# Kernel optimization log

Hardware: AMD Instinct MI355X
Metric: run time of the kernel (lower is better)

Reference implementation:

```python
import jax, jax.numpy as jnp
import numpy as np

N = 50000   # nodes
E = 800000  # edges (avg out-degree 16)
F = 64      # node features
HID = 128   # hidden size


def _seg(vals, idx, n):
    return jax.ops.segment_sum(vals, idx, num_segments=n)


def dconv(x, src, dst, nw_out, nw_in, W, b, n):
    # Diffusion convolution, K=2. W: (2, K, C, HID); directions: out-walk / in-walk.
    # k=0 term is the identity hop for both directions.
    h = x @ (W[0, 0] + W[1, 0])
    fwd = _seg(nw_out[:, None] * x[src], dst, n)  # (D_out^-1 A) x
    bwd = _seg(nw_in[:, None] * x[dst], src, n)   # (D_in^-1 A^T) x
    return h + fwd @ W[0, 1] + bwd @ W[1, 1] + b


def dcrnn_cell(x, src, dst, nw_out, nw_in, Wz, bz, Wr, br, Wh, bh, n, hid):
    # Single recurrent step with H initialized to zeros (as in the model's single-call use).
    h0 = jnp.zeros((x.shape[0], hid), x.dtype)
    xh = jnp.concatenate([x, h0], axis=-1)
    z = jax.nn.sigmoid(dconv(xh, src, dst, nw_out, nw_in, Wz, bz, n))
    r = jax.nn.sigmoid(dconv(xh, src, dst, nw_out, nw_in, Wr, br, n))
    xrh = jnp.concatenate([x, r * h0], axis=-1)
    h_tilde = jnp.tanh(dconv(xrh, src, dst, nw_out, nw_in, Wh, bh, n))
    return z * h0 + (1.0 - z) * h_tilde


def setup_inputs() -> dict:
    key = jax.random.key(0)
    ks = jax.random.split(key, 20)
    x = jax.random.normal(ks[0], (N, F), jnp.float32)
    edge_index = jax.random.randint(ks[1], (2, E), 0, N, jnp.int32)
    edge_weight = jax.random.uniform(ks[2], (E,), jnp.float32)

    c1 = F + HID
    c2 = HID + HID

    def mkW(k, c):
        return jax.random.normal(k, (2, 2, c, HID), jnp.float32) / np.float32(np.sqrt(c))

    inp = {
        "x": x,
        "edge_index": edge_index,
        "edge_weight": edge_weight,
        "W1_z": mkW(ks[3], c1), "b1_z": jnp.zeros((HID,), jnp.float32),
        "W1_r": mkW(ks[4], c1), "b1_r": jnp.zeros((HID,), jnp.float32),
        "W1_h": mkW(ks[5], c1), "b1_h": jnp.zeros((HID,), jnp.float32),
        "W2_z": mkW(ks[6], c2), "b2_z": jnp.zeros((HID,), jnp.float32),
        "W2_r": mkW(ks[7], c2), "b2_r": jnp.zeros((HID,), jnp.float32),
        "W2_h": mkW(ks[8], c2), "b2_h": jnp.zeros((HID,), jnp.float32),
        "Wlin": jax.random.normal(ks[9], (HID, 1), jnp.float32) / np.float32(np.sqrt(HID)),
        "blin": jnp.zeros((1,), jnp.float32),
    }
    return inp


def reference(x, edge_index, edge_weight,
              W1_z, b1_z, W1_r, b1_r, W1_h, b1_h,
              W2_z, b2_z, W2_r, b2_r, W2_h, b2_h,
              Wlin, blin):
    src, dst = edge_index[0], edge_index[1]
    n = x.shape[0]
    # Random-walk normalization of edge weights (out- and in-degree), safe reciprocal.
    deg_out = _seg(edge_weight, src, n)
    deg_in = _seg(edge_weight, dst, n)
    nw_out = edge_weight * jnp.where(deg_out[src] > 0, 1.0 / deg_out[src], 0.0)
    nw_in = edge_weight * jnp.where(deg_in[dst] > 0, 1.0 / deg_in[dst], 0.0)

    h = dcrnn_cell(x, src, dst, nw_out, nw_in, W1_z, b1_z, W1_r, b1_r, W1_h, b1_h, n, HID)
    h = dcrnn_cell(h, src, dst, nw_out, nw_in, W2_z, b2_z, W2_r, b2_r, W2_h, b2_h, n, HID)
    # dropout=0.0 -> identity; final linear head -> (N, 1)
    return h @ Wlin + blin
```

## Files before the change

### kernel.cpp

```cpp
#include <hip/hip_runtime.h>
#include <cstdint>
#include <type_traits>

#define NN 50000
#define NE 800000
#define CAP 48
#define NPART 391
#define BINCAP 2560
#define CHUNK 4096

typedef unsigned short u16;
typedef unsigned int u32;
typedef unsigned long long u64;
typedef u16 u16x8 __attribute__((ext_vector_type(8)));
typedef __bf16 bf16x8 __attribute__((ext_vector_type(8)));
typedef float f32x4 __attribute__((ext_vector_type(4)));

__device__ __forceinline__ u16 f2bf(float f) {
  u32 u = __float_as_uint(f);
  u = (u + 0x7fff + ((u >> 16) & 1)) >> 16;
  return (u16)u;
}
__device__ __forceinline__ float bf2f(u32 b) { return __uint_as_float(b << 16); }

__launch_bounds__(512)
__global__ void k_bin(const int* __restrict__ src, const int* __restrict__ dst,
                      const float* __restrict__ ew, int2* __restrict__ bins,
                      u32* __restrict__ binCnt) {
  const int dir = blockIdx.y;
  const int e0 = blockIdx.x * CHUNK;
  const int n = min(CHUNK, NE - e0);
  const int* key = dir ? src : dst;
  const int* oth = dir ? dst : src;
  __shared__ u32 cnt[512];
  __shared__ u32 scan[512];
  __shared__ u32 gbase[512];
  __shared__ int2 ent[CHUNK];
  __shared__ u32 dsts[CHUNK];
  const int t = threadIdx.x;
  cnt[t] = 0;
  __syncthreads();

  int pj[8], mj[8], wj[8];
  u32 oj[8];
#pragma unroll
  for (int j = 0; j < 8; ++j) {
    const int i = j * 512 + t;
    pj[j] = -1;
    if (i < n) {
      const int e = e0 + i;
      const int k = key[e];
      pj[j] = k >> 7;
      mj[j] = ((k & 127) << 16) | oth[e];
      wj[j] = __float_as_int(ew[e]);
      oj[j] = atomicAdd(&cnt[pj[j]], 1u);
    }
  }
  __syncthreads();
  scan[t] = cnt[t];
  __syncthreads();
  for (int s = 1; s < 512; s <<= 1) {
    u32 v = (t >= s) ? scan[t - s] : 0;
    __syncthreads();
    scan[t] += v;
    __syncthreads();
  }
  if (t < NPART) gbase[t] = cnt[t] ? atomicAdd(&binCnt[dir * NPART + t], cnt[t]) : 0;
  __syncthreads();
#pragma unroll
  for (int j = 0; j < 8; ++j) {
    if (pj[j] >= 0) {
      const int p = pj[j];
      const u32 slot = scan[p] - cnt[p] + oj[j];
      ent[slot] = make_int2(mj[j], wj[j]);
      const u32 go = gbase[p] + oj[j];
      dsts[slot] = (go < BINCAP) ? (u32)p * BINCAP + go : 0xFFFFFFFFu;
    }
  }
  __syncthreads();
  int2* bdir = bins + (size_t)dir * NPART * BINCAP;
  for (int i = t; i < n; i += 512) {
    const u32 d = dsts[i];
    if (d != 0xFFFFFFFFu) bdir[d] = ent[i];
  }
}

__launch_bounds__(512)
__global__ void k_scatter2(const int2* __restrict__ bins, const u32* __restrict__ binCnt,
                           int2* __restrict__ bucketF, int2* __restrict__ bucketB,
                           u32* __restrict__ cntNF, u32* __restrict__ cntNB,
                           float* __restrict__ invF, float* __restrict__ invB) {
  const int p = blockIdx.x, dir = blockIdx.y;
  __shared__ u64 cd[128];
  __shared__ int2 stage[128 * CAP];
  const int t = threadIdx.x;
  if (t < 128) cd[t] = 0;
  __syncthreads();
  const int2* bin = bins + ((size_t)dir * NPART + p) * BINCAP;
  int bn = binCnt[dir * NPART + p];
  if (bn > BINCAP) bn = BINCAP;
  for (int i = t; i < bn; i += 512) {
    const int2 e = bin[i];
    const int ln = e.x >> 16;
    const float w = __int_as_float(e.y);
    const u64 inc = (1ULL << 32) | (u64)__float2uint_rn(w * 16777216.0f);
    const u32 slot = (u32)(atomicAdd(&cd[ln], inc) >> 32);
    if (slot < CAP) stage[ln * CAP + slot] = make_int2(e.x & 0xffff, e.y);
  }
  __syncthreads();
  int2* bucket = dir ? bucketB : bucketF;
  for (int i = t; i < 128 * CAP; i += 512) {
    const int ln = i / CAP, s = i % CAP;
    const int g = p * 128 + ln;
    u32 c = (u32)(cd[ln] >> 32);
    if (c > CAP) c = CAP;
    if (g < NN && s < (int)c) bucket[(size_t)g * CAP + s] = stage[i];
  }
  if (t < 128) {
    const int g = p * 128 + t;
    if (g < NN) {
      u32 c = (u32)(cd[t] >> 32);
      const u32 dfix = (u32)cd[t];
      if (c > CAP) c = CAP;
      (dir ? cntNB : cntNF)[g] = c;
      (dir ? invB : invF)[g] = dfix ? 16777216.f / (float)dfix : 0.f;
    }
  }
}

__global__ void k_cast(const float* __restrict__ x, u16* __restrict__ xb) {
  int i = (blockIdx.x * 256 + threadIdx.x) * 8;
  if (i >= NN * 64) return;
  float4 v0 = *(const float4*)&x[i];
  float4 v1 = *(const float4*)&x[i + 4];
  u16x8 o;
  o[0] = f2bf(v0.x); o[1] = f2bf(v0.y); o[2] = f2bf(v0.z); o[3] = f2bf(v0.w);
  o[4] = f2bf(v1.x); o[5] = f2bf(v1.y); o[6] = f2bf(v1.z); o[7] = f2bf(v1.w);
  *(u16x8*)&xb[i] = o;
}

template <int C>
__global__ void k_pack(const float* __restrict__ Wz, const float* __restrict__ Wh,
                       u16* __restrict__ WpT) {
  constexpr int K = 3 * C;
  constexpr int CIN = (C == 64) ? 192 : 256;
  int col = blockIdx.x;
  int k = threadIdx.x;
  int part = k / C, c = k % C, o = col & 127;
  const float* W = (col < 128) ? Wz : Wh;
  float v;
  if (part == 0)      v = W[(0 * CIN + c) * 128 + o] + W[(2 * CIN + c) * 128 + o];
  else if (part == 1) v = W[(1 * CIN + c) * 128 + o];
  else                v = W[(3 * CIN + c) * 128 + o];
  WpT[col * K + k] = f2bf(v);
}

template <int C>
__launch_bounds__(256)
__global__ void k_gather(const u16* __restrict__ x, const u32* __restrict__ cntNF,
                         const int2* __restrict__ bucketF, const u32* __restrict__ cntNB,
                         const int2* __restrict__ bucketB, const float* __restrict__ invF,
                         const float* __restrict__ invB, u16* __restrict__ fwd,
                         u16* __restrict__ bwd) {
  constexpr int G = C / 8;
  constexpr int NG = 64 / G;
  const int node = blockIdx.x * 4 + (threadIdx.x >> 6);
  if (node >= NN) return;
  const int lane = threadIdx.x & 63;
  const int g = lane / G;
  const int p = lane % G;
  const uint4* xa = (const uint4*)x;

  const int nF = cntNF[node];
  const int nB = cntNB[node];

  int2 entF = make_int2(0, 0), entB = make_int2(0, 0);
  if (lane < nF) entF = bucketF[(size_t)node * CAP + lane];
  if (lane < nB) entB = bucketB[(size_t)node * CAP + lane];
  const float wFl = __int_as_float(entF.y) * invB[entF.x];
  const float wBl = __int_as_float(entB.y) * invF[entB.x];

  float accF[8], accB[8];
#pragma unroll
  for (int j = 0; j < 8; ++j) { accF[j] = 0.f; accB[j] = 0.f; }

  const int mm = nF > nB ? nF : nB;
#pragma unroll 2
  for (int i = 0; i < mm; i += NG) {
    const int ii = i + g;
    const int mF = __shfl(entF.x, ii);
    const float wF = __shfl(wFl, ii);
    const int mB = __shfl(entB.x, ii);
    const float wB = __shfl(wBl, ii);
    uint4 vF = {0, 0, 0, 0}, vB = {0, 0, 0, 0};
    if (ii < nF) vF = xa[(u32)mF * G + p];
    if (ii < nB) vB = xa[(u32)mB * G + p];
    accF[0] += wF * bf2f(vF.x & 0xffff); accF[1] += wF * bf2f(vF.x >> 16);
    accF[2] += wF * bf2f(vF.y & 0xffff); accF[3] += wF * bf2f(vF.y >> 16);
    accF[4] += wF * bf2f(vF.z & 0xffff); accF[5] += wF * bf2f(vF.z >> 16);
    accF[6] += wF * bf2f(vF.w & 0xffff); accF[7] += wF * bf2f(vF.w >> 16);
    accB[0] += wB * bf2f(vB.x & 0xffff); accB[1] += wB * bf2f(vB.x >> 16);
    accB[2] += wB * bf2f(vB.y & 0xffff); accB[3] += wB * bf2f(vB.y >> 16);
    accB[4] += wB * bf2f(vB.z & 0xffff); accB[5] += wB * bf2f(vB.z >> 16);
    accB[6] += wB * bf2f(vB.w & 0xffff); accB[7] += wB * bf2f(vB.w >> 16);
  }

#pragma unroll
  for (int s = 32; s >= G; s >>= 1) {
#pragma unroll
    for (int j = 0; j < 8; ++j) {
      accF[j] += __shfl_xor(accF[j], s);
      accB[j] += __shfl_xor(accB[j], s);
    }
  }

  if (g < 2) {
    const float* a = g ? accB : accF;
    u16* o = g ? bwd : fwd;
    u16x8 pv;
#pragma unroll
    for (int j = 0; j < 8; ++j) pv[j] = f2bf(a[j]);
    *(u16x8*)&o[(size_t)node * C + p * 8] = pv;
  }
}

template <int C, bool HEAD>
__launch_bounds__(256)
__global__ void k_gemm(const u16* __restrict__ P0, const u16* __restrict__ P1,
                       const u16* __restrict__ P2, const u16* __restrict__ WpT,
                       const float* __restrict__ bz, const float* __restrict__ bh,
                       void* __restrict__ outv, const float* __restrict__ wlin,
                       const float* __restrict__ blin) {
  constexpr int K = 3 * C;
  __shared__ char smem[40960];
  u16* As = (u16*)smem;
  u16* Bs = (u16*)(smem + 8192);
  const int t = threadIdx.x;
  const int w = t >> 6;
  const int l = t & 63;
  const int lc = l & 15, lq = l >> 4;
  const int bm = blockIdx.x * 64;

  f32x4 acc[4][4];
#pragma unroll
  for (int mi = 0; mi < 4; ++mi)
#pragma unroll
    for (int ni = 0; ni < 4; ++ni) acc[mi][ni] = (f32x4){0.f, 0.f, 0.f, 0.f};

  for (int kt = 0; kt < K / 64; ++kt) {
    const int k0 = kt * 64;
    const u16* P;
    int lc0;
    if (C == 64) { P = (kt == 0) ? P0 : (kt == 1 ? P1 : P2); lc0 = 0; }
    else         { P = (kt < 2) ? P0 : (kt < 4 ? P1 : P2);   lc0 = (kt & 1) * 64; }
    {
      const int row = t >> 2;
      const int gr = bm + row;
      const int g0 = (t & 3) * 2;
      u16x8 v0 = {0, 0, 0, 0, 0, 0, 0, 0}, v1 = v0;
      if (gr < NN) {
        const u16* s = &P[(size_t)gr * C + lc0 + g0 * 8];
        v0 = *(const u16x8*)s;
        v1 = *(const u16x8*)(s + 8);
      }
      *(u16x8*)&As[row * 64 + ((g0 ^ (row & 7)) * 8)] = v0;
      *(u16x8*)&As[row * 64 + (((g0 + 1) ^ (row & 7)) * 8)] = v1;
    }
    {
      const int col = t;
      const u16* s = &WpT[(size_t)col * K + k0];
#pragma unroll
      for (int g = 0; g < 8; ++g) {
        u16x8 v = *(const u16x8*)(s + g * 8);
        *(u16x8*)&Bs[col * 64 + ((g ^ (col & 7)) * 8)] = v;
      }
    }
    __syncthreads();
#pragma unroll
    for (int kk = 0; kk < 2; ++kk) {
      bf16x8 af[4], bfr[4];
#pragma unroll
      for (int mi = 0; mi < 4; ++mi) {
        const int row = 16 * mi + lc;
        const int g = kk * 4 + lq;
        af[mi] = *(const bf16x8*)&As[row * 64 + ((g ^ (row & 7)) * 8)];
      }
#pragma unroll
      for (int ni = 0; ni < 4; ++ni) {
        const int col = 64 * w + 16 * ni + lc;
        const int g = kk * 4 + lq;
        bfr[ni] = *(const bf16x8*)&Bs[col * 64 + ((g ^ (col & 7)) * 8)];
      }
#pragma unroll
      for (int mi = 0; mi < 4; ++mi)
#pragma unroll
        for (int ni = 0; ni < 4; ++ni)
          acc[mi][ni] = __builtin_amdgcn_mfma_f32_16x16x32_bf16(af[mi], bfr[ni],
                                                                acc[mi][ni], 0, 0, 0);
    }
    __syncthreads();
  }

  float* Hs = (float*)smem;
  if (w >= 2) {
#pragma unroll
    for (int mi = 0; mi < 4; ++mi)
#pragma unroll
      for (int ni = 0; ni < 4; ++ni) {
        const int c2 = 64 * (w - 2) + 16 * ni + lc;
        const float bhv = bh[c2];
#pragma unroll
        for (int r = 0; r < 4; ++r)
          Hs[(16 * mi + 4 * lq + r) * 129 + c2] = tanhf(acc[mi][ni][r] + bhv);
      }
  }
  float* outS = (float*)(smem + 33280);
  if (HEAD && t < 64) outS[t] = 0.f;
  __syncthreads();

  if (w < 2) {
    if constexpr (!HEAD) {
      u16* out = (u16*)outv;
#pragma unroll
      for (int mi = 0; mi < 4; ++mi)
#pragma unroll
        for (int ni = 0; ni < 4; ++ni) {
          const int col = 64 * w + 16 * ni + lc;
          const float bzv = bz[col];
#pragma unroll
          for (int r = 0; r < 4; ++r) {
            const int row = 16 * mi + 4 * lq + r;
            const int gr = bm + row;
            const float z = 1.f / (1.f + __expf(-(acc[mi][ni][r] + bzv)));
            const float hv = (1.f - z) * Hs[row * 129 + col];
            if (gr < NN) out[(size_t)gr * 128 + col] = f2bf(hv);
          }
        }
    } else {
#pragma unroll
      for (int mi = 0; mi < 4; ++mi)
#pragma unroll
        for (int r = 0; r < 4; ++r) {
          const int row = 16 * mi + 4 * lq + r;
          float part = 0.f;
#pragma unroll
          for (int ni = 0; ni < 4; ++ni) {
            const int col = 64 * w + 16 * ni + lc;
            const float z = 1.f / (1.f + __expf(-(acc[mi][ni][r] + bz[col])));
            part += (1.f - z) * Hs[row * 129 + col] * wlin[col];
          }
          part += __shfl_xor(part, 1);
          part += __shfl_xor(part, 2);
          part += __shfl_xor(part, 4);
          part += __shfl_xor(part, 8);
          if (lc == 0) atomicAdd(&outS[row], part);
        }
    }
  }
  if constexpr (HEAD) {
    __syncthreads();
    if (t < 64) {
      const int gr = bm + t;
      if (gr < NN) ((float*)outv)[gr] = outS[t] + blin[0];
    }
  }
}

extern "C" void kernel_launch(void* const* d_in, const int* in_sizes, int n_in,
                              void* d_out, int out_size, void* d_ws, size_t ws_size,
                              hipStream_t stream) {
  const float* x    = (const float*)d_in[0];
  const int*   ei   = (const int*)d_in[1];
  const float* ew   = (const float*)d_in[2];
  const float* W1z  = (const float*)d_in[3];
  const float* b1z  = (const float*)d_in[4];
  const float* W1h  = (const float*)d_in[7];
  const float* b1h  = (const float*)d_in[8];
  const float* W2z  = (const float*)d_in[9];
  const float* b2z  = (const float*)d_in[10];
  const float* W2h  = (const float*)d_in[13];
  const float* b2h  = (const float*)d_in[14];
  const float* Wlin = (const float*)d_in[15];
  const float* blin = (const float*)d_in[16];
  const int* src = ei;
  const int* dst = ei + NE;

  char* p8 = (char*)d_ws;
  auto alloc = [&](size_t bytes) { char* r = p8; p8 += (bytes + 15) & ~15ull; return r; };
  u32*   binCnt  = (u32*)alloc(2 * NPART * 4);
  int2*  bins    = (int2*)alloc((size_t)2 * NPART * BINCAP * 8);
  int2*  bucketF = (int2*)alloc((size_t)NN * CAP * 8);
  int2*  bucketB = (int2*)alloc((size_t)NN * CAP * 8);
  u32*   cntNF   = (u32*)alloc(NN * 4);
  u32*   cntNB   = (u32*)alloc(NN * 4);
  float* invF    = (float*)alloc(NN * 4);
  float* invB    = (float*)alloc(NN * 4);
  u16*   WpT1 = (u16*)alloc(256 * 192 * 2);
  u16*   WpT2 = (u16*)alloc(256 * 384 * 2);
  u16*   xb   = (u16*)alloc((size_t)NN * 64 * 2);
  u16*   h1   = (u16*)alloc((size_t)NN * 128 * 2);
  u16*   fwd1 = (u16*)alloc((size_t)NN * 64 * 2);
  u16*   bwd1 = (u16*)alloc((size_t)NN * 64 * 2);
  u16*   bwd2 = (u16*)alloc((size_t)NN * 128 * 2);
  u16*   fwd2 = fwd1;

  hipMemsetAsync(binCnt, 0, 2 * NPART * 4, stream);

  const dim3 binGrid((NE + CHUNK - 1) / CHUNK, 2);
  k_bin<<<binGrid, 512, 0, stream>>>(src, dst, ew, bins, binCnt);
  k_scatter2<<<dim3(NPART, 2), 512, 0, stream>>>(bins, binCnt, bucketF, bucketB,
                                                 cntNF, cntNB, invF, invB);
  k_pack<64><<<256, 192, 0, stream>>>(W1z, W1h, WpT1);
  k_pack<128><<<256, 384, 0, stream>>>(W2z, W2h, WpT2);
  k_cast<<<(NN * 64 / 8 + 255) / 256, 256, 0, stream>>>(x, xb);

  const int nb4 = (NN + 3) / 4;
  const int gblocks = (NN + 63) / 64;

  k_gather<64><<<nb4, 256, 0, stream>>>(xb, cntNF, bucketF, cntNB, bucketB, invF, invB,
                                        fwd1, bwd1);
  k_gemm<64, false><<<gblocks, 256, 0, stream>>>(xb, fwd1, bwd1, WpT1, b1z, b1h, h1,
                                                 nullptr, nullptr);
  k_gather<128><<<nb4, 256, 0, stream>>>(h1, cntNF, bucketF, cntNB, bucketB, invF, invB,
                                         fwd2, bwd2);
  k_gemm<128, true><<<gblocks, 256, 0, stream>>>(h1, fwd2, bwd2, WpT2, b2z, b2h,
                                                 d_out, Wlin, blin);
}
```

Before: 252.3 us.

## Sort gather neighbor lists per node and use persistent grid-stride gather blocks

Each wave now sorts its node's forward and backward neighbor entries by source index with an in-register 64-lane bitonic sort, so the feature-row gathers run in ascending address order for better cache and DRAM locality. Empty lanes are padded with a max key and clamped when indexing the inverse-degree arrays. The gather kernels also switch from one block per four nodes to a fixed grid of 1280 blocks looping over nodes. The sort adds about 21 shuffle stages per direction per node, and the different summation order changes bf16 rounding slightly.

```diff
diff --git a/kernel.cpp b/kernel.cpp
--- a/kernel.cpp
+++ b/kernel.cpp
@@ -8,6 +8,7 @@
 #define NPART 391
 #define BINCAP 2560
 #define CHUNK 4096
+#define NBLK 1280
 
 typedef unsigned short u16;
 typedef unsigned int u32;
@@ -22,6 +23,20 @@
   return (u16)u;
 }
 __device__ __forceinline__ float bf2f(u32 b) { return __uint_as_float(b << 16); }
+
+__device__ __forceinline__ void bitonic64(int& key, int& val, const int lane) {
+#pragma unroll
+  for (int k = 2; k <= 64; k <<= 1) {
+#pragma unroll
+    for (int j = k >> 1; j > 0; j >>= 1) {
+      const int pk = __shfl_xor(key, j);
+      const int pv = __shfl_xor(val, j);
+      const bool keepmin = ((lane & j) == 0) == ((lane & k) == 0);
+      const bool adopt = keepmin ? (pk < key) : (pk > key);
+      if (adopt) { key = pk; val = pv; }
+    }
+  }
+}
 
 __launch_bounds__(512)
 __global__ void k_bin(const int* __restrict__ src, const int* __restrict__ dst,
@@ -164,63 +179,69 @@
                          u16* __restrict__ bwd) {
   constexpr int G = C / 8;
   constexpr int NG = 64 / G;
-  const int node = blockIdx.x * 4 + (threadIdx.x >> 6);
-  if (node >= NN) return;
   const int lane = threadIdx.x & 63;
   const int g = lane / G;
   const int p = lane % G;
   const uint4* xa = (const uint4*)x;
 
-  const int nF = cntNF[node];
-  const int nB = cntNB[node];
-
-  int2 entF = make_int2(0, 0), entB = make_int2(0, 0);
-  if (lane < nF) entF = bucketF[(size_t)node * CAP + lane];
-  if (lane < nB) entB = bucketB[(size_t)node * CAP + lane];
-  const float wFl = __int_as_float(entF.y) * invB[entF.x];
-  const float wBl = __int_as_float(entB.y) * invF[entB.x];
-
-  float accF[8], accB[8];
-#pragma unroll
-  for (int j = 0; j < 8; ++j) { accF[j] = 0.f; accB[j] = 0.f; }
-
-  const int mm = nF > nB ? nF : nB;
+  for (int node = blockIdx.x * 4 + (threadIdx.x >> 6); node < NN; node += NBLK * 4) {
+    const int nF = cntNF[node];
+    const int nB = cntNB[node];
+
+    int2 entF = make_int2(0x7FFFFFFF, 0), entB = make_int2(0x7FFFFFFF, 0);
+    if (lane < nF) entF = bucketF[(size_t)node * CAP + lane];
+    if (lane < nB) entB = bucketB[(size_t)node * CAP + lane];
+
+    bitonic64(entF.x, entF.y, lane);
+    bitonic64(entB.x, entB.y, lane);
+
+    const int ixF = min(entF.x, NN - 1);
+    const int ixB = min(entB.x, NN - 1);
+    const float wFl = __int_as_float(entF.y) * invB[ixF];
+    const float wBl = __int_as_float(entB.y) * invF[ixB];
+
+    float accF[8], accB[8];
+#pragma unroll
+    for (int j = 0; j < 8; ++j) { accF[j] = 0.f; accB[j] = 0.f; }
+
+    const int mm = nF > nB ? nF : nB;
 #pragma unroll 2
-  for (int i = 0; i < mm; i += NG) {
-    const int ii = i + g;
-    const int mF = __shfl(entF.x, ii);
-    const float wF = __shfl(wFl, ii);
-    const int mB = __shfl(entB.x, ii);
-    const float wB = __shfl(wBl, ii);
-    uint4 vF = {0, 0, 0, 0}, vB = {0, 0, 0, 0};
-    if (ii < nF) vF = xa[(u32)mF * G + p];
-    if (ii < nB) vB = xa[(u32)mB * G + p];
-    accF[0] += wF * bf2f(vF.x & 0xffff); accF[1] += wF * bf2f(vF.x >> 16);
-    accF[2] += wF * bf2f(vF.y & 0xffff); accF[3] += wF * bf2f(vF.y >> 16);
-    accF[4] += wF * bf2f(vF.z & 0xffff); accF[5] += wF * bf2f(vF.z >> 16);
-    accF[6] += wF * bf2f(vF.w & 0xffff); accF[7] += wF * bf2f(vF.w >> 16);
-    accB[0] += wB * bf2f(vB.x & 0xffff); accB[1] += wB * bf2f(vB.x >> 16);
-    accB[2] += wB * bf2f(vB.y & 0xffff); accB[3] += wB * bf2f(vB.y >> 16);
-    accB[4] += wB * bf2f(vB.z & 0xffff); accB[5] += wB * bf2f(vB.z >> 16);
-    accB[6] += wB * bf2f(vB.w & 0xffff); accB[7] += wB * bf2f(vB.w >> 16);
-  }
-
-#pragma unroll
-  for (int s = 32; s >= G; s >>= 1) {
-#pragma unroll
-    for (int j = 0; j < 8; ++j) {
-      accF[j] += __shfl_xor(accF[j], s);
-      accB[j] += __shfl_xor(accB[j], s);
-    }
-  }
-
-  if (g < 2) {
-    const float* a = g ? accB : accF;
-    u16* o = g ? bwd : fwd;
-    u16x8 pv;
-#pragma unroll
-    for (int j = 0; j < 8; ++j) pv[j] = f2bf(a[j]);
-    *(u16x8*)&o[(size_t)node * C + p * 8] = pv;
+    for (int i = 0; i < mm; i += NG) {
+      const int ii = i + g;
+      const int mF = __shfl(entF.x, ii);
+      const float wF = __shfl(wFl, ii);
+      const int mB = __shfl(entB.x, ii);
+      const float wB = __shfl(wBl, ii);
+      uint4 vF = {0, 0, 0, 0}, vB = {0, 0, 0, 0};
+      if (ii < nF) vF = xa[(u32)mF * G + p];
+      if (ii < nB) vB = xa[(u32)mB * G + p];
+      accF[0] += wF * bf2f(vF.x & 0xffff); accF[1] += wF * bf2f(vF.x >> 16);
+      accF[2] += wF * bf2f(vF.y & 0xffff); accF[3] += wF * bf2f(vF.y >> 16);
+      accF[4] += wF * bf2f(vF.z & 0xffff); accF[5] += wF * bf2f(vF.z >> 16);
+      accF[6] += wF * bf2f(vF.w & 0xffff); accF[7] += wF * bf2f(vF.w >> 16);
+      accB[0] += wB * bf2f(vB.x & 0xffff); accB[1] += wB * bf2f(vB.x >> 16);
+      accB[2] += wB * bf2f(vB.y & 0xffff); accB[3] += wB * bf2f(vB.y >> 16);
+      accB[4] += wB * bf2f(vB.z & 0xffff); accB[5] += wB * bf2f(vB.z >> 16);
+      accB[6] += wB * bf2f(vB.w & 0xffff); accB[7] += wB * bf2f(vB.w >> 16);
+    }
+
+#pragma unroll
+    for (int s = 32; s >= G; s >>= 1) {
+#pragma unroll
+      for (int j = 0; j < 8; ++j) {
+        accF[j] += __shfl_xor(accF[j], s);
+        accB[j] += __shfl_xor(accB[j], s);
+      }
+    }
+
+    if (g < 2) {
+      const float* a = g ? accB : accF;
+      u16* o = g ? bwd : fwd;
+      u16x8 pv;
+#pragma unroll
+      for (int j = 0; j < 8; ++j) pv[j] = f2bf(a[j]);
+      *(u16x8*)&o[(size_t)node * C + p * 8] = pv;
+    }
   }
 }
 
@@ -414,15 +435,14 @@
   k_pack<128><<<256, 384, 0, stream>>>(W2z, W2h, WpT2);
   k_cast<<<(NN * 64 / 8 + 255) / 256, 256, 0, stream>>>(x, xb);
 
-  const int nb4 = (NN + 3) / 4;
   const int gblocks = (NN + 63) / 64;
 
-  k_gather<64><<<nb4, 256, 0, stream>>>(xb, cntNF, bucketF, cntNB, bucketB, invF, invB,
-                                        fwd1, bwd1);
+  k_gather<64><<<NBLK, 256, 0, stream>>>(xb, cntNF, bucketF, cntNB, bucketB, invF, invB,
+                                         fwd1, bwd1);
   k_gemm<64, false><<<gblocks, 256, 0, stream>>>(xb, fwd1, bwd1, WpT1, b1z, b1h, h1,
                                                  nullptr, nullptr);
-  k_gather<128><<<nb4, 256, 0, stream>>>(h1, cntNF, bucketF, cntNB, bucketB, invF, invB,
-                                         fwd2, bwd2);
+  k_gather<128><<<NBLK, 256, 0, stream>>>(h1, cntNF, bucketF, cntNB, bucketB, invF, invB,
+                                          fwd2, bwd2);
   k_gemm<128, true><<<gblocks, 256, 0, stream>>>(h1, fwd2, bwd2, WpT2, b2z, b2h,
                                                  d_out, Wlin, blin);
 }
```

New measurement: 317.5 us. 25.8% more time.

## Pack bucket entries into 32-bit index+fp16 weight and widen GEMM tile to 128 rows

Applied to the files above, without the earlier changes.

Bucket entries shrink from 8-byte int2 (index, float weight) to a 32-bit word holding a 16-bit local index and an fp16 weight. This halves bucket write and read traffic in the scatter and gather kernels, and the gather now reads buckets with nontemporal loads. The GEMM block tile doubles from 64 to 128 rows, so each B tile load is reused by more MFMAs, with the epilogue run in two 64-row halves. The costs are reduced weight precision, more accumulator registers (possibly lower occupancy), and a larger shared-memory footprint.

```diff
diff --git a/kernel.cpp b/kernel.cpp
--- a/kernel.cpp
+++ b/kernel.cpp
@@ -1,4 +1,5 @@
 #include <hip/hip_runtime.h>
+#include <hip/hip_fp16.h>
 #include <cstdint>
 #include <type_traits>
 
@@ -87,12 +88,12 @@
 
 __launch_bounds__(512)
 __global__ void k_scatter2(const int2* __restrict__ bins, const u32* __restrict__ binCnt,
-                           int2* __restrict__ bucketF, int2* __restrict__ bucketB,
+                           u32* __restrict__ bucketF, u32* __restrict__ bucketB,
                            u32* __restrict__ cntNF, u32* __restrict__ cntNB,
                            float* __restrict__ invF, float* __restrict__ invB) {
   const int p = blockIdx.x, dir = blockIdx.y;
   __shared__ u64 cd[128];
-  __shared__ int2 stage[128 * CAP];
+  __shared__ u32 stage[128 * CAP];
   const int t = threadIdx.x;
   if (t < 128) cd[t] = 0;
   __syncthreads();
@@ -105,10 +106,12 @@
     const float w = __int_as_float(e.y);
     const u64 inc = (1ULL << 32) | (u64)__float2uint_rn(w * 16777216.0f);
     const u32 slot = (u32)(atomicAdd(&cd[ln], inc) >> 32);
-    if (slot < CAP) stage[ln * CAP + slot] = make_int2(e.x & 0xffff, e.y);
-  }
-  __syncthreads();
-  int2* bucket = dir ? bucketB : bucketF;
+    const __half hw = __float2half_rn(w);
+    if (slot < CAP)
+      stage[ln * CAP + slot] = ((u32)(e.x & 0xffff) << 16) | (u32)__half_as_ushort(hw);
+  }
+  __syncthreads();
+  u32* bucket = dir ? bucketB : bucketF;
   for (int i = t; i < 128 * CAP; i += 512) {
     const int ln = i / CAP, s = i % CAP;
     const int g = p * 128 + ln;
@@ -158,8 +161,8 @@
 template <int C>
 __launch_bounds__(256)
 __global__ void k_gather(const u16* __restrict__ x, const u32* __restrict__ cntNF,
-                         const int2* __restrict__ bucketF, const u32* __restrict__ cntNB,
-                         const int2* __restrict__ bucketB, const float* __restrict__ invF,
+                         const u32* __restrict__ bucketF, const u32* __restrict__ cntNB,
+                         const u32* __restrict__ bucketB, const float* __restrict__ invF,
                          const float* __restrict__ invB, u16* __restrict__ fwd,
                          u16* __restrict__ bwd) {
   constexpr int G = C / 8;
@@ -174,11 +177,15 @@
   const int nF = cntNF[node];
   const int nB = cntNB[node];
 
-  int2 entF = make_int2(0, 0), entB = make_int2(0, 0);
-  if (lane < nF) entF = bucketF[(size_t)node * CAP + lane];
-  if (lane < nB) entB = bucketB[(size_t)node * CAP + lane];
-  const float wFl = __int_as_float(entF.y) * invB[entF.x];
-  const float wBl = __int_as_float(entB.y) * invF[entB.x];
+  u32 eF = 0, eB = 0;
+  if (lane < nF) eF = __builtin_nontemporal_load(&bucketF[(size_t)node * CAP + lane]);
+  if (lane < nB) eB = __builtin_nontemporal_load(&bucketB[(size_t)node * CAP + lane]);
+  const int idxF = eF >> 16;
+  const int idxB = eB >> 16;
+  const float wFl =
+      __half2float(__ushort_as_half((u16)(eF & 0xffff))) * invB[idxF];
+  const float wBl =
+      __half2float(__ushort_as_half((u16)(eB & 0xffff))) * invF[idxB];
 
   float accF[8], accB[8];
 #pragma unroll
@@ -188,9 +195,9 @@
 #pragma unroll 2
   for (int i = 0; i < mm; i += NG) {
     const int ii = i + g;
-    const int mF = __shfl(entF.x, ii);
+    const int mF = __shfl(idxF, ii);
     const float wF = __shfl(wFl, ii);
-    const int mB = __shfl(entB.x, ii);
+    const int mB = __shfl(idxB, ii);
     const float wB = __shfl(wBl, ii);
     uint4 vF = {0, 0, 0, 0}, vB = {0, 0, 0, 0};
     if (ii < nF) vF = xa[(u32)mF * G + p];
@@ -232,18 +239,18 @@
                        void* __restrict__ outv, const float* __restrict__ wlin,
                        const float* __restrict__ blin) {
   constexpr int K = 3 * C;
-  __shared__ char smem[40960];
+  __shared__ char smem[49152];
   u16* As = (u16*)smem;
-  u16* Bs = (u16*)(smem + 8192);
+  u16* Bs = (u16*)(smem + 16384);
   const int t = threadIdx.x;
   const int w = t >> 6;
   const int l = t & 63;
   const int lc = l & 15, lq = l >> 4;
-  const int bm = blockIdx.x * 64;
-
-  f32x4 acc[4][4];
-#pragma unroll
-  for (int mi = 0; mi < 4; ++mi)
+  const int bm = blockIdx.x * 128;
+
+  f32x4 acc[8][4];
+#pragma unroll
+  for (int mi = 0; mi < 8; ++mi)
 #pragma unroll
     for (int ni = 0; ni < 4; ++ni) acc[mi][ni] = (f32x4){0.f, 0.f, 0.f, 0.f};
 
@@ -254,17 +261,20 @@
     if (C == 64) { P = (kt == 0) ? P0 : (kt == 1 ? P1 : P2); lc0 = 0; }
     else         { P = (kt < 2) ? P0 : (kt < 4 ? P1 : P2);   lc0 = (kt & 1) * 64; }
     {
-      const int row = t >> 2;
+      const int row = t >> 1;
       const int gr = bm + row;
-      const int g0 = (t & 3) * 2;
-      u16x8 v0 = {0, 0, 0, 0, 0, 0, 0, 0}, v1 = v0;
+      const int g0 = (t & 1) * 4;
+      u16x8 v[4];
+#pragma unroll
+      for (int j = 0; j < 4; ++j) v[j] = (u16x8){0, 0, 0, 0, 0, 0, 0, 0};
       if (gr < NN) {
         const u16* s = &P[(size_t)gr * C + lc0 + g0 * 8];
-        v0 = *(const u16x8*)s;
-        v1 = *(const u16x8*)(s + 8);
-      }
-      *(u16x8*)&As[row * 64 + ((g0 ^ (row & 7)) * 8)] = v0;
-      *(u16x8*)&As[row * 64 + (((g0 + 1) ^ (row & 7)) * 8)] = v1;
+#pragma unroll
+        for (int j = 0; j < 4; ++j) v[j] = *(const u16x8*)(s + j * 8);
+      }
+#pragma unroll
+      for (int j = 0; j < 4; ++j)
+        *(u16x8*)&As[row * 64 + (((g0 + j) ^ (row & 7)) * 8)] = v[j];
     }
     {
       const int col = t;
@@ -278,9 +288,9 @@
     __syncthreads();
 #pragma unroll
     for (int kk = 0; kk < 2; ++kk) {
-      bf16x8 af[4], bfr[4];
-#pragma unroll
-      for (int mi = 0; mi < 4; ++mi) {
+      bf16x8 af[8], bfr[4];
+#pragma unroll
+      for (int mi = 0; mi < 8; ++mi) {
         const int row = 16 * mi + lc;
         const int g = kk * 4 + lq;
         af[mi] = *(const bf16x8*)&As[row * 64 + ((g ^ (row & 7)) * 8)];
@@ -292,7 +302,7 @@
         bfr[ni] = *(const bf16x8*)&Bs[col * 64 + ((g ^ (col & 7)) * 8)];
       }
 #pragma unroll
-      for (int mi = 0; mi < 4; ++mi)
+      for (int mi = 0; mi < 8; ++mi)
 #pragma unroll
         for (int ni = 0; ni < 4; ++ni)
           acc[mi][ni] = __builtin_amdgcn_mfma_f32_16x16x32_bf16(af[mi], bfr[ni],
@@ -302,67 +312,74 @@
   }
 
   float* Hs = (float*)smem;
-  if (w >= 2) {
-#pragma unroll
-    for (int mi = 0; mi < 4; ++mi)
-#pragma unroll
-      for (int ni = 0; ni < 4; ++ni) {
-        const int c2 = 64 * (w - 2) + 16 * ni + lc;
-        const float bhv = bh[c2];
-#pragma unroll
-        for (int r = 0; r < 4; ++r)
-          Hs[(16 * mi + 4 * lq + r) * 129 + c2] = tanhf(acc[mi][ni][r] + bhv);
-      }
-  }
   float* outS = (float*)(smem + 33280);
-  if (HEAD && t < 64) outS[t] = 0.f;
-  __syncthreads();
-
-  if (w < 2) {
-    if constexpr (!HEAD) {
-      u16* out = (u16*)outv;
+#pragma unroll
+  for (int half = 0; half < 2; ++half) {
+    if (w >= 2) {
 #pragma unroll
       for (int mi = 0; mi < 4; ++mi)
 #pragma unroll
         for (int ni = 0; ni < 4; ++ni) {
-          const int col = 64 * w + 16 * ni + lc;
-          const float bzv = bz[col];
+          const int c2 = 64 * (w - 2) + 16 * ni + lc;
+          const float bhv = bh[c2];
+#pragma unroll
+          for (int r = 0; r < 4; ++r)
+            Hs[(16 * mi + 4 * lq + r) * 129 + c2] =
+                tanhf(acc[4 * half + mi][ni][r] + bhv);
+        }
+    }
+    if (HEAD && t < 64) outS[t] = 0.f;
+    __syncthreads();
+
+    if (w < 2) {
+      if constexpr (!HEAD) {
+        u16* out = (u16*)outv;
+#pragma unroll
+        for (int mi = 0; mi < 4; ++mi)
+#pragma unroll
+          for (int ni = 0; ni < 4; ++ni) {
+            const int col = 64 * w + 16 * ni + lc;
+            const float bzv = bz[col];
+#pragma unroll
+            for (int r = 0; r < 4; ++r) {
+              const int row = 16 * mi + 4 * lq + r;
+              const int gr = bm + 64 * half + row;
+              const float z =
+                  1.f / (1.f + __expf(-(acc[4 * half + mi][ni][r] + bzv)));
+              const float hv = (1.f - z) * Hs[row * 129 + col];
+              if (gr < NN) out[(size_t)gr * 128 + col] = f2bf(hv);
+            }
+          }
+      } else {
+#pragma unroll
+        for (int mi = 0; mi < 4; ++mi)
 #pragma unroll
           for (int r = 0; r < 4; ++r) {
             const int row = 16 * mi + 4 * lq + r;
-            const int gr = bm + row;
-            const float z = 1.f / (1.f + __expf(-(acc[mi][ni][r] + bzv)));
-            const float hv = (1.f - z) * Hs[row * 129 + col];
-            if (gr < NN) out[(size_t)gr * 128 + col] = f2bf(hv);
+            float part = 0.f;
+#pragma unroll
+            for (int ni = 0; ni < 4; ++ni) {
+              const int col = 64 * w + 16 * ni + lc;
+              const float z =
+                  1.f / (1.f + __expf(-(acc[4 * half + mi][ni][r] + bz[col])));
+              part += (1.f - z) * Hs[row * 129 + col] * wlin[col];
+            }
+            part += __shfl_xor(part, 1);
+            part += __shfl_xor(part, 2);
+            part += __shfl_xor(part, 4);
+            part += __shfl_xor(part, 8);
+            if (lc == 0) atomicAdd(&outS[row], part);
           }
-        }
-    } else {
-#pragma unroll
-      for (int mi = 0; mi < 4; ++mi)
-#pragma unroll
-        for (int r = 0; r < 4; ++r) {
-          const int row = 16 * mi + 4 * lq + r;
-          float part = 0.f;
-#pragma unroll
-          for (int ni = 0; ni < 4; ++ni) {
-            const int col = 64 * w + 16 * ni + lc;
-            const float z = 1.f / (1.f + __expf(-(acc[mi][ni][r] + bz[col])));
-            part += (1.f - z) * Hs[row * 129 + col] * wlin[col];
-          }
-          part += __shfl_xor(part, 1);
-          part += __shfl_xor(part, 2);
-          part += __shfl_xor(part, 4);
-          part += __shfl_xor(part, 8);
-          if (lc == 0) atomicAdd(&outS[row], part);
-        }
-    }
-  }
-  if constexpr (HEAD) {
-    __syncthreads();
-    if (t < 64) {
-      const int gr = bm + t;
-      if (gr < NN) ((float*)outv)[gr] = outS[t] + blin[0];
-    }
+      }
+    }
+    if constexpr (HEAD) {
+      __syncthreads();
+      if (t < 64) {
+        const int gr = bm + 64 * half + t;
+        if (gr < NN) ((float*)outv)[gr] = outS[t] + blin[0];
+      }
+    }
+    __syncthreads();
   }
 }
 
@@ -389,8 +406,8 @@
   auto alloc = [&](size_t bytes) { char* r = p8; p8 += (bytes + 15) & ~15ull; return r; };
   u32*   binCnt  = (u32*)alloc(2 * NPART * 4);
   int2*  bins    = (int2*)alloc((size_t)2 * NPART * BINCAP * 8);
-  int2*  bucketF = (int2*)alloc((size_t)NN * CAP * 8);
-  int2*  bucketB = (int2*)alloc((size_t)NN * CAP * 8);
+  u32*   bucketF = (u32*)alloc((size_t)NN * CAP * 4);
+  u32*   bucketB = (u32*)alloc((size_t)NN * CAP * 4);
   u32*   cntNF   = (u32*)alloc(NN * 4);
   u32*   cntNB   = (u32*)alloc(NN * 4);
   float* invF    = (float*)alloc(NN * 4);
@@ -415,7 +432,7 @@
   k_cast<<<(NN * 64 / 8 + 255) / 256, 256, 0, stream>>>(x, xb);
 
   const int nb4 = (NN + 3) / 4;
-  const int gblocks = (NN + 63) / 64;
+  const int gblocks = (NN + 127) / 128;
 
   k_gather<64><<<nb4, 256, 0, stream>>>(xb, cntNF, bucketF, cntNB, bucketB, invF, invB,
                                         fwd1, bwd1);
```

Result: slower. 314.5 us (+24.6%).
